# Kernel optimization log

Hardware: AMD Instinct MI355X
Metric: run time of the kernel (lower is better)

Reference implementation:

```python
import jax, jax.numpy as jnp
import numpy as np

N_NODES = 100000


def gcn_conv(x, edge_index, W, b):
    # PyG GCNConv: add self-loops, symmetric normalization D^-1/2 (A+I) D^-1/2, transform, aggregate, bias.
    src, dst = edge_index[0], edge_index[1]
    n = x.shape[0]
    xw = x @ W  # [N, out] transform before propagate (PyG order)
    # degree with self-loops (count edges by target + 1)
    deg = jax.ops.segment_sum(jnp.ones_like(dst, dtype=xw.dtype), dst, num_segments=n) + 1.0
    dinv = jax.lax.rsqrt(deg)  # deg >= 1, safe
    norm = dinv[src] * dinv[dst]  # [E]
    msgs = xw[src] * norm[:, None]  # [E, out] gathered, normalized messages
    agg = jax.ops.segment_sum(msgs, dst, num_segments=n)
    # self-loop contribution: norm_ii = dinv_i^2 = 1/deg_i
    agg = agg + xw * (dinv * dinv)[:, None]
    return agg + b


def setup_inputs() -> dict:
    key = jax.random.key(0)
    ks = jax.random.split(key, 8)
    in_c, h1, h2, out_c = 128, 71, 82, 1
    x = jax.random.normal(ks[0], (N_NODES, in_c), dtype=jnp.float32)
    edge_index = jax.random.randint(ks[1], (2, 1600000), 0, N_NODES, dtype=jnp.int64)
    def glorot(k, fan_in, fan_out):
        s = jnp.sqrt(6.0 / (fan_in + fan_out))
        return jax.random.uniform(k, (fan_in, fan_out), jnp.float32, -s, s)
    return {
        "x": x,
        "edge_index": edge_index,
        "W1": glorot(ks[2], in_c, h1), "b1": jnp.zeros((h1,), jnp.float32),
        "W2": glorot(ks[3], h1, h2), "b2": jnp.zeros((h2,), jnp.float32),
        "W3": glorot(ks[4], h2, out_c), "b3": jnp.zeros((out_c,), jnp.float32),
    }


def reference(x, edge_index, W1, b1, W2, b2, W3, b3):
    h = jax.nn.relu(gcn_conv(x, edge_index, W1, b1))
    h = gcn_conv(h, edge_index, W2, b2)  # note: no relu after conv2 in source
    return gcn_conv(h, edge_index, W3, b3)
```

## Files before the change

kernel.cpp:

```cpp
#include <hip/hip_runtime.h>
#include <hip/hip_fp16.h>

#define NNODES 100000
#define NB 391
#define BSHIFT 8
#define BMASK 255
#define BCAP 4864
#define WT_LD 136

typedef _Float16 half8 __attribute__((ext_vector_type(8)));
typedef float floatx4 __attribute__((ext_vector_type(4)));

__global__ __launch_bounds__(1024) void binAP_kernel(
        const int* __restrict__ src, const int* __restrict__ dst,
        int* __restrict__ bcnt, unsigned* __restrict__ bdata, int E,
        const float* __restrict__ W1, const float* __restrict__ W2,
        const float* __restrict__ b2, const float* __restrict__ W3,
        float* __restrict__ w23, __half* __restrict__ Wt) {
    if (blockIdx.x == NB) {
        int k = threadIdx.x;
        if (k < 71) {
            float a = 0.f;
            for (int j = 0; j < 82; ++j) a += W2[k * 82 + j] * W3[j];
            w23[k] = a;
        } else if (k == 71) {
            float a = 0.f;
            for (int j = 0; j < 82; ++j) a += b2[j] * W3[j];
            w23[71] = a;
        }
        for (int i = threadIdx.x; i < 80 * WT_LD; i += 1024) {
            int nn = i / WT_LD, kk = i - nn * WT_LD;
            float v = (nn < 71 && kk < 128) ? W1[kk * 71 + nn] : 0.f;
            Wt[i] = __float2half(v);
        }
        return;
    }
    __shared__ int hist[NB];
    __shared__ int gb[NB];
    __shared__ int cur[NB];
    const int BATCH = 4096;
    int tid = threadIdx.x;
    for (int base = blockIdx.x * BATCH; base < E; base += NB * BATCH) {
        for (int i = tid; i < NB; i += 1024) hist[i] = 0;
        __syncthreads();
        int s[4], d[4];
        int cnt = 0;
        if (base + BATCH <= E) {
            int4 sv = ((const int4*)(src + base))[tid];
            int4 dv = ((const int4*)(dst + base))[tid];
            s[cnt] = sv.x; d[cnt] = dv.x; atomicAdd(&hist[dv.x >> BSHIFT], 1); ++cnt;
            s[cnt] = sv.y; d[cnt] = dv.y; atomicAdd(&hist[dv.y >> BSHIFT], 1); ++cnt;
            s[cnt] = sv.z; d[cnt] = dv.z; atomicAdd(&hist[dv.z >> BSHIFT], 1); ++cnt;
            s[cnt] = sv.w; d[cnt] = dv.w; atomicAdd(&hist[dv.w >> BSHIFT], 1); ++cnt;
        } else {
#pragma unroll
            for (int k = 0; k < 4; ++k) {
                int idx = base + k * 1024 + tid;
                if (idx < E) {
                    s[cnt] = src[idx];
                    d[cnt] = dst[idx];
                    atomicAdd(&hist[d[cnt] >> BSHIFT], 1);
                    ++cnt;
                }
            }
        }
        __syncthreads();
        for (int i = tid; i < NB; i += 1024) {
            int c = hist[i];
            gb[i] = (c > 0) ? atomicAdd(&bcnt[i], c) : 0;
            cur[i] = 0;
        }
        __syncthreads();
        for (int k = 0; k < cnt; ++k) {
            int b = d[k] >> BSHIFT;
            int lo = gb[b] + atomicAdd(&cur[b], 1);
            if (lo < BCAP)
                bdata[(size_t)b * BCAP + lo] = ((unsigned)s[k] << BSHIFT) | ((unsigned)d[k] & BMASK);
        }
        __syncthreads();
    }
}

__global__ __launch_bounds__(1024) void binB2_kernel(
        const int* __restrict__ bcnt, const unsigned* __restrict__ bdata,
        int* __restrict__ deg, int* __restrict__ end_off, float* __restrict__ dinv,
        int* __restrict__ csr, int n) {
    __shared__ unsigned edata[BCAP];
    __shared__ int hist[256];
    __shared__ int cur[256];
    __shared__ int wsum[4];
    __shared__ int scal[2];
    int b = blockIdx.x;
    int tid = threadIdx.x;
    if (tid < 64) {
        int s = 0;
        int lo = tid * 7, hi = min(tid * 7 + 7, b);
        for (int i = lo; i < hi; ++i) s += min(bcnt[i], BCAP);
#pragma unroll
        for (int off = 32; off; off >>= 1) s += __shfl_down(s, off);
        if (tid == 0) { scal[0] = s; scal[1] = min(bcnt[b], BCAP); }
    }
    if (tid < 256) hist[tid] = 0;
    __syncthreads();
    int cnt = scal[1];
    int base = scal[0];
    const unsigned* p = bdata + (size_t)b * BCAP;
    for (int i = tid; i < cnt; i += 1024) {
        unsigned e = p[i];
        edata[i] = e;
        atomicAdd(&hist[e & BMASK], 1);
    }
    __syncthreads();
    if (tid < 256) {
        int v = hist[tid];
        int lane = tid & 63;
        int incl = v;
#pragma unroll
        for (int off = 1; off < 64; off <<= 1) {
            int t = __shfl_up(incl, off);
            if (lane >= off) incl += t;
        }
        cur[tid] = incl;
        if (lane == 63) wsum[tid >> 6] = incl;
    }
    __syncthreads();
    if (tid == 0) {
        int acc = 0;
#pragma unroll
        for (int w = 0; w < 4; ++w) { int t = wsum[w]; wsum[w] = acc; acc += t; }
    }
    __syncthreads();
    if (tid < 256) {
        int v = hist[tid];
        int start = base + wsum[tid >> 6] + cur[tid] - v;
        int node = (b << BSHIFT) + tid;
        if (node < n) {
            deg[node] = v;
            end_off[node] = start + v;
            dinv[node] = rsqrtf((float)v + 1.0f);
        }
        cur[tid] = start;
    }
    __syncthreads();
    for (int i = tid; i < cnt; i += 1024) {
        unsigned e = edata[i];
        int pos = atomicAdd(&cur[e & BMASK], 1);
        csr[pos] = (int)(e >> BSHIFT);
    }
}

__global__ __launch_bounds__(256) void xform_mfma(
        const float* __restrict__ x, const __half* __restrict__ Wt,
        const float* __restrict__ scale, __half* __restrict__ msgA,
        __half* __restrict__ msgB, int n) {
    __shared__ __half Wsh[80 * WT_LD];
    {
        const uint4* sp = (const uint4*)Wt;
        uint4* dp = (uint4*)Wsh;
        for (int i = threadIdx.x; i < (80 * WT_LD * 2) / 16; i += blockDim.x) dp[i] = sp[i];
    }
    __syncthreads();
    int lane = threadIdx.x & 63;
    int m = lane & 15, q = lane >> 4;
    int gw = (blockIdx.x * blockDim.x + threadIdx.x) >> 6;
    int nw = (gridDim.x * blockDim.x) >> 6;
    int nrt = n >> 4;
    for (int rt = gw; rt < nrt; rt += nw) {
        int rb = rt << 4;
        const float* xr = x + (size_t)(rb + m) * 128 + q * 8;
        floatx4 acc[5];
#pragma unroll
        for (int t = 0; t < 5; ++t) acc[t] = (floatx4){0.f, 0.f, 0.f, 0.f};
#pragma unroll
        for (int ks = 0; ks < 4; ++ks) {
            float4 f0 = *(const float4*)(xr + ks * 32);
            float4 f1 = *(const float4*)(xr + ks * 32 + 4);
            half8 a;
            a[0] = (_Float16)f0.x; a[1] = (_Float16)f0.y;
            a[2] = (_Float16)f0.z; a[3] = (_Float16)f0.w;
            a[4] = (_Float16)f1.x; a[5] = (_Float16)f1.y;
            a[6] = (_Float16)f1.z; a[7] = (_Float16)f1.w;
#pragma unroll
            for (int t = 0; t < 5; ++t) {
                half8 b = *(const half8*)&Wsh[(t * 16 + m) * WT_LD + ks * 32 + q * 8];
                acc[t] = __builtin_amdgcn_mfma_f32_16x16x32_f16(a, b, acc[t], 0, 0, 0);
            }
        }
        float sc[4];
#pragma unroll
        for (int r = 0; r < 4; ++r) sc[r] = scale[rb + q * 4 + r];
#pragma unroll
        for (int t = 0; t < 5; ++t) {
            int col = t * 16 + m;
#pragma unroll
            for (int r = 0; r < 4; ++r) {
                __half hv = __float2half(acc[t][r] * sc[r]);
                int row = rb + q * 4 + r;
                if (t < 4) {
                    msgA[(size_t)row * 64 + col] = hv;
                } else if (m < 8) {
                    msgB[(size_t)row * 8 + m] = hv;
                }
            }
        }
    }
}

__global__ __launch_bounds__(256) void gather_fused(
        const __half* __restrict__ msgA, const __half* __restrict__ msgB,
        const int* __restrict__ csr, const int* __restrict__ end_off,
        const int* __restrict__ deg, const float* __restrict__ dinv,
        const float* __restrict__ b, const float* __restrict__ w23,
        float* __restrict__ g2, int n) {
    int lane = threadIdx.x & 63;
    int li = lane & 7;
    int wid = (blockIdx.x * blockDim.x + threadIdx.x) >> 6;
    int nwaves = (gridDim.x * blockDim.x) >> 6;
    float bA[8], wA[8];
#pragma unroll
    for (int j = 0; j < 8; ++j) { bA[j] = b[8 * li + j]; wA[j] = w23[8 * li + j]; }
    float bB = (li < 7) ? b[64 + li] : 0.f;
    float wB = (li < 7) ? w23[64 + li] : 0.f;
    const char* mA = (const char*)msgA;
    const char* mB = (const char*)msgB;
    unsigned laneA   = (unsigned)(li << 4);
    unsigned laneBof = (unsigned)((li >> 1) << 2);
    unsigned laneBsh = (unsigned)((li & 1) << 4);
    int ntiles = n >> 3;
    for (int tile = wid; tile < ntiles; tile += nwaves) {
        int node = (tile << 3) + (lane >> 3);
        int ee = end_off[node];
        int d = deg[node];
        int st = ee - d;
        float dv = dinv[node];
        int tmax = d;
        tmax = max(tmax, __shfl_xor(tmax, 8));
        tmax = max(tmax, __shfl_xor(tmax, 16));
        tmax = max(tmax, __shfl_xor(tmax, 32));
        tmax = __builtin_amdgcn_readfirstlane(tmax);
        float acc[8];
#pragma unroll
        for (int j = 0; j < 8; ++j) acc[j] = 0.f;
        float bsum = 0.f;
        int c0 = csr[(0 < d) ? st + 0 : 0];
        int c1 = csr[(1 < d) ? st + 1 : 0];
        int c2 = csr[(2 < d) ? st + 2 : 0];
        int c3 = csr[(3 < d) ? st + 3 : 0];
        int c4 = csr[(4 < d) ? st + 4 : 0];
        int c5 = csr[(5 < d) ? st + 5 : 0];
        int c6 = csr[(6 < d) ? st + 6 : 0];
        int c7 = csr[(7 < d) ? st + 7 : 0];
        unsigned i0 = (unsigned)((0 < d) ? c0 : node);
        unsigned i1 = (unsigned)((1 < d) ? c1 : node);
        unsigned i2 = (unsigned)((2 < d) ? c2 : node);
        unsigned i3 = (unsigned)((3 < d) ? c3 : node);
        half8 r0 = *(const half8*)(mA + ((i0 << 7) | laneA));
        half8 r1 = *(const half8*)(mA + ((i1 << 7) | laneA));
        half8 r2 = *(const half8*)(mA + ((i2 << 7) | laneA));
        half8 r3 = *(const half8*)(mA + ((i3 << 7) | laneA));
        unsigned w0 = *(const unsigned*)(mB + ((i0 << 4) | laneBof));
        unsigned w1 = *(const unsigned*)(mB + ((i1 << 4) | laneBof));
        unsigned w2 = *(const unsigned*)(mB + ((i2 << 4) | laneBof));
        unsigned w3 = *(const unsigned*)(mB + ((i3 << 4) | laneBof));
        for (int i = 0; i <= tmax; i += 4) {
            int n0 = csr[(i + 8  < d) ? st + i + 8  : 0];
            int n1 = csr[(i + 9  < d) ? st + i + 9  : 0];
            int n2 = csr[(i + 10 < d) ? st + i + 10 : 0];
            int n3 = csr[(i + 11 < d) ? st + i + 11 : 0];
            unsigned j0 = (unsigned)((i + 4 < d) ? c4 : node);
            unsigned j1 = (unsigned)((i + 5 < d) ? c5 : node);
            unsigned j2 = (unsigned)((i + 6 < d) ? c6 : node);
            unsigned j3 = (unsigned)((i + 7 < d) ? c7 : node);
            half8 s0 = *(const half8*)(mA + ((j0 << 7) | laneA));
            half8 s1 = *(const half8*)(mA + ((j1 << 7) | laneA));
            half8 s2 = *(const half8*)(mA + ((j2 << 7) | laneA));
            half8 s3 = *(const half8*)(mA + ((j3 << 7) | laneA));
            unsigned u0 = *(const unsigned*)(mB + ((j0 << 4) | laneBof));
            unsigned u1 = *(const unsigned*)(mB + ((j1 << 4) | laneBof));
            unsigned u2 = *(const unsigned*)(mB + ((j2 << 4) | laneBof));
            unsigned u3 = *(const unsigned*)(mB + ((j3 << 4) | laneBof));
            if (i <= d) {
#pragma unroll
                for (int j = 0; j < 8; ++j) acc[j] += (float)r0[j];
                unsigned short us = (unsigned short)(w0 >> laneBsh);
                _Float16 hf; __builtin_memcpy(&hf, &us, 2);
                bsum += (float)hf;
            }
            if (i + 1 <= d) {
#pragma unroll
                for (int j = 0; j < 8; ++j) acc[j] += (float)r1[j];
                unsigned short us = (unsigned short)(w1 >> laneBsh);
                _Float16 hf; __builtin_memcpy(&hf, &us, 2);
                bsum += (float)hf;
            }
            if (i + 2 <= d) {
#pragma unroll
                for (int j = 0; j < 8; ++j) acc[j] += (float)r2[j];
                unsigned short us = (unsigned short)(w2 >> laneBsh);
                _Float16 hf; __builtin_memcpy(&hf, &us, 2);
                bsum += (float)hf;
            }
            if (i + 3 <= d) {
#pragma unroll
                for (int j = 0; j < 8; ++j) acc[j] += (float)r3[j];
                unsigned short us = (unsigned short)(w3 >> laneBsh);
                _Float16 hf; __builtin_memcpy(&hf, &us, 2);
                bsum += (float)hf;
            }
            c4 = n0; c5 = n1; c6 = n2; c7 = n3;
            r0 = s0; r1 = s1; r2 = s2; r3 = s3;
            w0 = u0; w1 = u1; w2 = u2; w3 = u3;
        }
        float p = 0.f;
#pragma unroll
        for (int j = 0; j < 8; ++j) p += fmaxf(dv * acc[j] + bA[j], 0.f) * wA[j];
        p += fmaxf(dv * bsum + bB, 0.f) * wB;
        p += __shfl_xor(p, 1);
        p += __shfl_xor(p, 2);
        p += __shfl_xor(p, 4);
        if (li == 0) g2[node] = dv * p;
    }
}

__global__ void sgather_q(const float* __restrict__ g2, const int* __restrict__ csr,
                          const int* __restrict__ end_off, const int* __restrict__ deg,
                          const float* __restrict__ dinv, const float* __restrict__ w23,
                          float* __restrict__ q, int n) {
    float bw = w23[71];
    int lane = threadIdx.x & 63;
    int g = lane >> 4, k = lane & 15;
    int wid = (blockIdx.x * blockDim.x + threadIdx.x) >> 6;
    int nw = (gridDim.x * blockDim.x) >> 6;
    for (int i0 = wid * 4; i0 < n; i0 += nw * 4) {
        int i = i0 + g;
        float acc = 0.f;
        float dv = 0.f;
        if (i < n) {
            int end = end_off[i];
            int cnt = deg[i];
            int start = end - cnt;
            dv = dinv[i];
            int e = k;
            for (; e + 16 < cnt; e += 32) {
                int a0 = csr[start + e];
                int a1 = csr[start + e + 16];
                acc += g2[a0] + g2[a1];
            }
            for (; e < cnt; e += 16) acc += g2[csr[start + e]];
        }
        acc += __shfl_down(acc, 8, 16);
        acc += __shfl_down(acc, 4, 16);
        acc += __shfl_down(acc, 2, 16);
        acc += __shfl_down(acc, 1, 16);
        if (i < n && k == 0) q[i] = dv * (dv * (acc + g2[i]) + bw);
    }
}

__global__ void sgather_out(const float* __restrict__ q, const int* __restrict__ csr,
                            const int* __restrict__ end_off, const int* __restrict__ deg,
                            const float* __restrict__ dinv, const float* __restrict__ b3,
                            float* __restrict__ out, int n) {
    float bv = b3[0];
    int lane = threadIdx.x & 63;
    int g = lane >> 4, k = lane & 15;
    int wid = (blockIdx.x * blockDim.x + threadIdx.x) >> 6;
    int nw = (gridDim.x * blockDim.x) >> 6;
    for (int i0 = wid * 4; i0 < n; i0 += nw * 4) {
        int i = i0 + g;
        float acc = 0.f;
        float dv = 0.f;
        if (i < n) {
            int end = end_off[i];
            int cnt = deg[i];
            int start = end - cnt;
            dv = dinv[i];
            int e = k;
            for (; e + 16 < cnt; e += 32) {
                int a0 = csr[start + e];
                int a1 = csr[start + e + 16];
                acc += q[a0] + q[a1];
            }
            for (; e < cnt; e += 16) acc += q[csr[start + e]];
        }
        acc += __shfl_down(acc, 8, 16);
        acc += __shfl_down(acc, 4, 16);
        acc += __shfl_down(acc, 2, 16);
        acc += __shfl_down(acc, 1, 16);
        if (i < n && k == 0) out[i] = dv * (acc + q[i]) + bv;
    }
}

extern "C" void kernel_launch(void* const* d_in, const int* in_sizes, int n_in,
                              void* d_out, int out_size, void* d_ws, size_t ws_size,
                              hipStream_t stream) {
    const float* x  = (const float*)d_in[0];
    const int*   ei = (const int*)d_in[1];
    const float* W1 = (const float*)d_in[2];
    const float* b1 = (const float*)d_in[3];
    const float* W2 = (const float*)d_in[4];
    const float* b2 = (const float*)d_in[5];
    const float* W3 = (const float*)d_in[6];
    const float* b3 = (const float*)d_in[7];
    float* out = (float*)d_out;

    const int n = NNODES;
    const int E = in_sizes[1] / 2;
    const int* src = ei;
    const int* dst = ei + E;

    float* ws     = (float*)d_ws;
    float* dinv   = ws;
    int*   deg_i  = (int*)(ws + n);
    int*   offs   = deg_i + n;
    int*   bcnt   = offs + n;
    float* w23    = (float*)(bcnt + 512);
    __half* Wt    = (__half*)(w23 + 80);
    float* g2     = (float*)(Wt + 11008);
    float* q      = g2 + n;
    int*   csr    = (int*)(q + n);
    __half* msgA  = (__half*)(csr + E + 16);
    __half* msgB  = msgA + (size_t)n * 64;
    unsigned* bdata = (unsigned*)(msgB + (size_t)n * 8);

    hipMemsetAsync(bcnt, 0, 512 * sizeof(int), stream);
    binAP_kernel<<<NB + 1, 1024, 0, stream>>>(src, dst, bcnt, bdata, E,
                                              W1, W2, b2, W3, w23, Wt);
    binB2_kernel<<<NB, 1024, 0, stream>>>(bcnt, bdata, deg_i, offs, dinv, csr, n);
    xform_mfma<<<1563, 256, 0, stream>>>(x, Wt, dinv, msgA, msgB, n);
    gather_fused<<<3125, 256, 0, stream>>>(msgA, msgB, csr, offs, deg_i, dinv, b1, w23, g2, n);
    sgather_q<<<2048, 256, 0, stream>>>(g2, csr, offs, deg_i, dinv, w23, q, n);
    sgather_out<<<2048, 256, 0, stream>>>(q, csr, offs, deg_i, dinv, b3, out, n);
}
```

Before: 206.1 us.

## Locally sort edges in shared memory before coalesced scatter to bins and CSR

Both binning kernels now record each edge's atomic rank during the histogram pass, then place edges into a shared-memory sorted buffer using an exclusive scan. The global writes to bucket storage and to the CSR array become contiguous runs instead of scattered per-edge writes. The second shared atomic pass is also removed. In exchange the kernels use more shared memory, add extra barriers and scan steps, and keep per-thread rank registers. The CSR kernel assumes at most five edges per thread, which BCAP of 4864 with 1024 threads satisfies.

```diff
diff --git a/kernel.cpp b/kernel.cpp
--- a/kernel.cpp
+++ b/kernel.cpp
@@ -35,23 +35,31 @@
         }
         return;
     }
+    __shared__ unsigned sorted[4096];
+    __shared__ unsigned short bkt[4096];
     __shared__ int hist[NB];
+    __shared__ int sbase[NB];
     __shared__ int gb[NB];
-    __shared__ int cur[NB];
+    __shared__ int wsum[8];
+    int tid = threadIdx.x;
     const int BATCH = 4096;
-    int tid = threadIdx.x;
     for (int base = blockIdx.x * BATCH; base < E; base += NB * BATCH) {
+        int bE = min(BATCH, E - base);
         for (int i = tid; i < NB; i += 1024) hist[i] = 0;
         __syncthreads();
-        int s[4], d[4];
+        int s[4], d[4], rk[4], bb[4];
         int cnt = 0;
-        if (base + BATCH <= E) {
+        if (bE == BATCH) {
             int4 sv = ((const int4*)(src + base))[tid];
             int4 dv = ((const int4*)(dst + base))[tid];
-            s[cnt] = sv.x; d[cnt] = dv.x; atomicAdd(&hist[dv.x >> BSHIFT], 1); ++cnt;
-            s[cnt] = sv.y; d[cnt] = dv.y; atomicAdd(&hist[dv.y >> BSHIFT], 1); ++cnt;
-            s[cnt] = sv.z; d[cnt] = dv.z; atomicAdd(&hist[dv.z >> BSHIFT], 1); ++cnt;
-            s[cnt] = sv.w; d[cnt] = dv.w; atomicAdd(&hist[dv.w >> BSHIFT], 1); ++cnt;
+            s[0] = sv.x; d[0] = dv.x; s[1] = sv.y; d[1] = dv.y;
+            s[2] = sv.z; d[2] = dv.z; s[3] = sv.w; d[3] = dv.w;
+            cnt = 4;
+#pragma unroll
+            for (int k = 0; k < 4; ++k) {
+                bb[k] = d[k] >> BSHIFT;
+                rk[k] = atomicAdd(&hist[bb[k]], 1);
+            }
         } else {
 #pragma unroll
             for (int k = 0; k < 4; ++k) {
@@ -59,23 +67,49 @@
                 if (idx < E) {
                     s[cnt] = src[idx];
                     d[cnt] = dst[idx];
-                    atomicAdd(&hist[d[cnt] >> BSHIFT], 1);
+                    bb[cnt] = d[cnt] >> BSHIFT;
+                    rk[cnt] = atomicAdd(&hist[bb[cnt]], 1);
                     ++cnt;
                 }
             }
         }
         __syncthreads();
-        for (int i = tid; i < NB; i += 1024) {
-            int c = hist[i];
-            gb[i] = (c > 0) ? atomicAdd(&bcnt[i], c) : 0;
-            cur[i] = 0;
+        if (tid < 448) {
+            int v = (tid < NB) ? hist[tid] : 0;
+            int lane = tid & 63;
+            int incl = v;
+#pragma unroll
+            for (int off = 1; off < 64; off <<= 1) {
+                int t = __shfl_up(incl, off);
+                if (lane >= off) incl += t;
+            }
+            if (tid < NB) sbase[tid] = incl - v;
+            if (lane == 63) wsum[tid >> 6] = incl;
+        }
+        __syncthreads();
+        if (tid == 0) {
+            int acc = 0;
+#pragma unroll
+            for (int w = 0; w < 7; ++w) { int t = wsum[w]; wsum[w] = acc; acc += t; }
+        }
+        __syncthreads();
+        if (tid < NB) {
+            sbase[tid] += wsum[tid >> 6];
+            int c = hist[tid];
+            gb[tid] = (c > 0) ? atomicAdd(&bcnt[tid], c) : 0;
         }
         __syncthreads();
         for (int k = 0; k < cnt; ++k) {
-            int b = d[k] >> BSHIFT;
-            int lo = gb[b] + atomicAdd(&cur[b], 1);
+            int pos = sbase[bb[k]] + rk[k];
+            sorted[pos] = ((unsigned)s[k] << BSHIFT) | ((unsigned)d[k] & BMASK);
+            bkt[pos] = (unsigned short)bb[k];
+        }
+        __syncthreads();
+        for (int i = tid; i < bE; i += 1024) {
+            int bb2 = bkt[i];
+            int lo = gb[bb2] + (i - sbase[bb2]);
             if (lo < BCAP)
-                bdata[(size_t)b * BCAP + lo] = ((unsigned)s[k] << BSHIFT) | ((unsigned)d[k] & BMASK);
+                bdata[(size_t)bb2 * BCAP + lo] = sorted[i];
         }
         __syncthreads();
     }
@@ -85,9 +119,9 @@
         const int* __restrict__ bcnt, const unsigned* __restrict__ bdata,
         int* __restrict__ deg, int* __restrict__ end_off, float* __restrict__ dinv,
         int* __restrict__ csr, int n) {
-    __shared__ unsigned edata[BCAP];
+    __shared__ unsigned sorted[BCAP];
     __shared__ int hist[256];
-    __shared__ int cur[256];
+    __shared__ int nstart[256];
     __shared__ int wsum[4];
     __shared__ int scal[2];
     int b = blockIdx.x;
@@ -105,10 +139,13 @@
     int cnt = scal[1];
     int base = scal[0];
     const unsigned* p = bdata + (size_t)b * BCAP;
+    unsigned ev[5]; int rv[5];
+    int ec = 0;
     for (int i = tid; i < cnt; i += 1024) {
         unsigned e = p[i];
-        edata[i] = e;
-        atomicAdd(&hist[e & BMASK], 1);
+        ev[ec] = e;
+        rv[ec] = atomicAdd(&hist[e & BMASK], 1);
+        ++ec;
     }
     __syncthreads();
     if (tid < 256) {
@@ -120,7 +157,7 @@
             int t = __shfl_up(incl, off);
             if (lane >= off) incl += t;
         }
-        cur[tid] = incl;
+        nstart[tid] = incl - v;
         if (lane == 63) wsum[tid >> 6] = incl;
     }
     __syncthreads();
@@ -131,22 +168,23 @@
     }
     __syncthreads();
     if (tid < 256) {
+        int excl = nstart[tid] + wsum[tid >> 6];
+        nstart[tid] = excl;
         int v = hist[tid];
-        int start = base + wsum[tid >> 6] + cur[tid] - v;
         int node = (b << BSHIFT) + tid;
         if (node < n) {
             deg[node] = v;
-            end_off[node] = start + v;
+            end_off[node] = base + excl + v;
             dinv[node] = rsqrtf((float)v + 1.0f);
         }
-        cur[tid] = start;
-    }
-    __syncthreads();
-    for (int i = tid; i < cnt; i += 1024) {
-        unsigned e = edata[i];
-        int pos = atomicAdd(&cur[e & BMASK], 1);
-        csr[pos] = (int)(e >> BSHIFT);
-    }
+    }
+    __syncthreads();
+    for (int k = 0; k < ec; ++k) {
+        unsigned e = ev[k];
+        sorted[nstart[e & BMASK] + rv[k]] = e >> BSHIFT;
+    }
+    __syncthreads();
+    for (int i = tid; i < cnt; i += 1024) csr[base + i] = (int)sorted[i];
 }
 
 __global__ __launch_bounds__(256) void xform_mfma(
```

After: 200.5 us, median of 2. 2.7% less time.
